# Optimization experiments

Hardware: AMD Instinct MI355X
Metric: run time of the kernel (lower is better)

Reference implementation:

```python
import jax, jax.numpy as jnp
import numpy as np

SYM_LIST = jnp.array([0, 1, 2, 3])  # init kwarg sym_list


def setup_inputs() -> dict:
    key = jax.random.key(0)
    k1, k2, k3, k4 = jax.random.split(key, 4)
    bs, n = 16, 2048
    target = jax.random.normal(k1, (bs, n, 3), dtype=jnp.float32)
    model_points = jax.random.normal(k2, (bs, n, 3), dtype=jnp.float32)
    idx = jax.random.randint(k3, (bs, 1), 0, 8)
    H = jax.random.normal(k4, (bs, 4, 4), dtype=jnp.float32)
    return {"target": target, "model_points": model_points, "idx": idx, "H": H}


def reference(target, model_points, idx, H):
    # base = H[:, :3, :3]^T per batch; pred = model_points @ base + t
    base = jnp.swapaxes(H[:, :3, :3], 1, 2)            # [bs, 3, 3]
    t = H[:, :3, 3][:, None, :]                        # [bs, 1, 3]
    tf = jnp.einsum('bnd,bde->bne', model_points, base) + t  # [bs, N, 3]

    # Squared pairwise distances (argmin-equivalent to L2 norm used in knn()).
    # d2[b, q, r] = ||tf[b,q] - target[b,r]||^2
    d2 = (jnp.sum(tf * tf, axis=-1)[:, :, None]
          + jnp.sum(target * target, axis=-1)[:, None, :]
          - 2.0 * jnp.einsum('bqd,brd->bqr', tf, target))  # [bs, N, N]
    inds = jnp.argmin(d2, axis=2)                      # [bs, N] nearest target per query
    gathered = jnp.take_along_axis(target, inds[:, :, None], axis=1)  # [bs, N, 3]

    # Only symmetric objects (idx in sym_list) get the NN-rearranged target.
    is_sym = jnp.isin(idx[:, 0], SYM_LIST)[:, None, None]  # [bs, 1, 1]
    tgt = jnp.where(is_sym, gathered, target)

    # dis = mean_n ||tf - tgt||_2, per batch element
    dis = jnp.mean(jnp.linalg.norm(tf - tgt, axis=2), axis=1)  # [bs]
    return dis
```

## Files before the change

### kernel.cpp

```cpp
#include <hip/hip_runtime.h>

#define N 2048
#define BS 16
#define QG 256
#define NQG (N / QG)
#define TS 256
#define NTS (N / TS)
#define WAVES 4
#define TPB (WAVES * 64)
#define TPW (TS / WAVES)


__global__ __launch_bounds__(TPB) void addsloss_k1(
    const float* __restrict__ target,
    const float* __restrict__ mp,
    const int* __restrict__ idx,
    const float* __restrict__ H,
    float* __restrict__ wsmin)
{
    __shared__ float4 tlds[TS];
    __shared__ float  pmin[WAVES][QG];

    const int bid  = blockIdx.x;
    const int b    = bid >> 6;
    const int rem  = bid & 63;
    const int qg   = rem >> 3;
    const int ts   = rem & 7;
    const int tid  = threadIdx.x;
    const int wave = tid >> 6;
    const int lane = tid & 63;

    const int  cls = idx[b];
    const bool sym = (cls >= 0) && (cls <= 3);
    if (!sym) return;

    const float* tb = target + (size_t)b * N * 3;
    const float* mb = mp     + (size_t)b * N * 3;
    const float* hb = H      + b * 16;

    {
        const int t = ts * TS + tid;
        const float x = tb[t * 3 + 0];
        const float y = tb[t * 3 + 1];
        const float z = tb[t * 3 + 2];
        tlds[tid] = make_float4(x, y, z, x * x + y * y + z * z);
    }

    float fx[4], fy[4], fz[4];
    #pragma unroll
    for (int qi = 0; qi < 4; ++qi) {
        const int q = qg * QG + qi * 64 + lane;
        const float m0 = mb[q * 3 + 0];
        const float m1 = mb[q * 3 + 1];
        const float m2 = mb[q * 3 + 2];
        fx[qi] = hb[0] * m0 + hb[1]  * m1 + hb[2]  * m2 + hb[3];
        fy[qi] = hb[4] * m0 + hb[5]  * m1 + hb[6]  * m2 + hb[7];
        fz[qi] = hb[8] * m0 + hb[9]  * m1 + hb[10] * m2 + hb[11];
    }

    __syncthreads();

    const float4* t4 = &tlds[wave * TPW];

    float acc[4][4];
    #pragma unroll
    for (int qi = 0; qi < 4; ++qi)
        #pragma unroll
        for (int ti = 0; ti < 4; ++ti) acc[qi][ti] = 3.4e38f;

    for (int j = 0; j < TPW; j += 4) {
        const float4 T0 = t4[j + 0];
        const float4 T1 = t4[j + 1];
        const float4 T2 = t4[j + 2];
        const float4 T3 = t4[j + 3];
        #pragma unroll
        for (int qi = 0; qi < 4; ++qi) {
            float dot;
            dot = T0.x * fx[qi]; dot = fmaf(T0.y, fy[qi], dot); dot = fmaf(T0.z, fz[qi], dot);
            acc[qi][0] = fminf(acc[qi][0], fmaf(dot, -2.0f, T0.w));
            dot = T1.x * fx[qi]; dot = fmaf(T1.y, fy[qi], dot); dot = fmaf(T1.z, fz[qi], dot);
            acc[qi][1] = fminf(acc[qi][1], fmaf(dot, -2.0f, T1.w));
            dot = T2.x * fx[qi]; dot = fmaf(T2.y, fy[qi], dot); dot = fmaf(T2.z, fz[qi], dot);
            acc[qi][2] = fminf(acc[qi][2], fmaf(dot, -2.0f, T2.w));
            dot = T3.x * fx[qi]; dot = fmaf(T3.y, fy[qi], dot); dot = fmaf(T3.z, fz[qi], dot);
            acc[qi][3] = fminf(acc[qi][3], fmaf(dot, -2.0f, T3.w));
        }
    }

    #pragma unroll
    for (int qi = 0; qi < 4; ++qi)
        pmin[wave][qi * 64 + lane] =
            fminf(fminf(acc[qi][0], acc[qi][1]), fminf(acc[qi][2], acc[qi][3]));
    __syncthreads();

    float* wrow = wsmin + ((size_t)(b * NTS + ts)) * N + qg * QG;
    const float m = fminf(fminf(pmin[0][tid], pmin[1][tid]),
                          fminf(pmin[2][tid], pmin[3][tid]));
    wrow[tid] = m;
}

__global__ __launch_bounds__(1024) void addsloss_k2(
    const float* __restrict__ target,
    const float* __restrict__ mp,
    const int* __restrict__ idx,
    const float* __restrict__ H,
    const float* __restrict__ wsmin,
    float* __restrict__ out)
{
    __shared__ float ps[16];
    const int b    = blockIdx.x;
    const int tid  = threadIdx.x;
    const int wave = tid >> 6;
    const int lane = tid & 63;

    const int  cls = idx[b];
    const bool sym = (cls >= 0) && (cls <= 3);

    const float* tb = target + (size_t)b * N * 3;
    const float* mb = mp     + (size_t)b * N * 3;
    const float* hb = H      + b * 16;

    float s = 0.0f;
    #pragma unroll
    for (int k = 0; k < N / 1024; ++k) {
        const int q = k * 1024 + tid;
        const float m0 = mb[q * 3 + 0];
        const float m1 = mb[q * 3 + 1];
        const float m2 = mb[q * 3 + 2];
        const float fx = hb[0] * m0 + hb[1]  * m1 + hb[2]  * m2 + hb[3];
        const float fy = hb[4] * m0 + hb[5]  * m1 + hb[6]  * m2 + hb[7];
        const float fz = hb[8] * m0 + hb[9]  * m1 + hb[10] * m2 + hb[11];

        float d;
        if (sym) {
            float m = 3.4e38f;
            #pragma unroll
            for (int t = 0; t < NTS; ++t)
                m = fminf(m, wsmin[((size_t)(b * NTS + t)) * N + q]);
            const float c = fx * fx + fy * fy + fz * fz;
            d = sqrtf(fmaxf(0.0f, c + m));
        } else {
            const float dx = fx - tb[q * 3 + 0];
            const float dy = fy - tb[q * 3 + 1];
            const float dz = fz - tb[q * 3 + 2];
            d = sqrtf(dx * dx + dy * dy + dz * dz);
        }
        s += d;
    }

    #pragma unroll
    for (int off = 32; off > 0; off >>= 1) s += __shfl_down(s, off);
    if (lane == 0) ps[wave] = s;
    __syncthreads();
    if (tid == 0) {
        float tot = 0.0f;
        #pragma unroll
        for (int w = 0; w < 16; ++w) tot += ps[w];
        out[b] = tot * (1.0f / (float)N);
    }
}

extern "C" void kernel_launch(void* const* d_in, const int* in_sizes, int n_in,
                              void* d_out, int out_size, void* d_ws, size_t ws_size,
                              hipStream_t stream) {
    const float* target = (const float*)d_in[0];
    const float* mp     = (const float*)d_in[1];
    const int*   idx    = (const int*)  d_in[2];
    const float* H      = (const float*)d_in[3];
    float*       out    = (float*)d_out;
    float*       wsmin  = (float*)d_ws;

    addsloss_k1<<<BS * NQG * NTS, TPB, 0, stream>>>(target, mp, idx, H, wsmin);
    addsloss_k2<<<BS, 1024, 0, stream>>>(target, mp, idx, H, wsmin, out);
}
```

Before: 15.51 us.

## Halve target tile to double k1 blocks, fold -2 factor, vectorize k2 loads

The target tile size drops from 256 to 128, which doubles the k1 grid to 2048 blocks so more work runs in parallel across CUs. The -2 scale is folded into the query coordinates so each distance takes three FMAs with no extra multiply, and the inner loop is fully unrolled. k2 now runs 512 threads that each handle 4 queries, using float4 loads for the points and the partial minima. The trade-off is twice as many partial-min rows (16 per query) to write and reduce, plus half-idle threads when staging target points into shared memory.

Measured after the change: 14.58 us. 1.06x faster.

```diff
diff --git a/kernel.cpp b/kernel.cpp
--- a/kernel.cpp
+++ b/kernel.cpp
@@ -4,11 +4,12 @@
 #define BS 16
 #define QG 256
 #define NQG (N / QG)
-#define TS 256
+#define TS 128
 #define NTS (N / TS)
 #define WAVES 4
 #define TPB (WAVES * 64)
 #define TPW (TS / WAVES)
+#define F4I (TPW / 4)
 
 
 __global__ __launch_bounds__(TPB) void addsloss_k1(
@@ -22,10 +23,10 @@
     __shared__ float  pmin[WAVES][QG];
 
     const int bid  = blockIdx.x;
-    const int b    = bid >> 6;
-    const int rem  = bid & 63;
-    const int qg   = rem >> 3;
-    const int ts   = rem & 7;
+    const int b    = bid >> 7;
+    const int rem  = bid & 127;
+    const int qg   = rem >> 4;
+    const int ts   = rem & 15;
     const int tid  = threadIdx.x;
     const int wave = tid >> 6;
     const int lane = tid & 63;
@@ -38,7 +39,7 @@
     const float* mb = mp     + (size_t)b * N * 3;
     const float* hb = H      + b * 16;
 
-    {
+    if (tid < TS) {
         const int t = ts * TS + tid;
         const float x = tb[t * 3 + 0];
         const float y = tb[t * 3 + 1];
@@ -46,16 +47,16 @@
         tlds[tid] = make_float4(x, y, z, x * x + y * y + z * z);
     }
 
-    float fx[4], fy[4], fz[4];
+    float ngx[4], ngy[4], ngz[4];
     #pragma unroll
     for (int qi = 0; qi < 4; ++qi) {
         const int q = qg * QG + qi * 64 + lane;
         const float m0 = mb[q * 3 + 0];
         const float m1 = mb[q * 3 + 1];
         const float m2 = mb[q * 3 + 2];
-        fx[qi] = hb[0] * m0 + hb[1]  * m1 + hb[2]  * m2 + hb[3];
-        fy[qi] = hb[4] * m0 + hb[5]  * m1 + hb[6]  * m2 + hb[7];
-        fz[qi] = hb[8] * m0 + hb[9]  * m1 + hb[10] * m2 + hb[11];
+        ngx[qi] = -2.0f * (hb[0] * m0 + hb[1]  * m1 + hb[2]  * m2 + hb[3]);
+        ngy[qi] = -2.0f * (hb[4] * m0 + hb[5]  * m1 + hb[6]  * m2 + hb[7]);
+        ngz[qi] = -2.0f * (hb[8] * m0 + hb[9]  * m1 + hb[10] * m2 + hb[11]);
     }
 
     __syncthreads();
@@ -68,22 +69,23 @@
         #pragma unroll
         for (int ti = 0; ti < 4; ++ti) acc[qi][ti] = 3.4e38f;
 
-    for (int j = 0; j < TPW; j += 4) {
-        const float4 T0 = t4[j + 0];
-        const float4 T1 = t4[j + 1];
-        const float4 T2 = t4[j + 2];
-        const float4 T3 = t4[j + 3];
+    #pragma unroll
+    for (int j = 0; j < F4I; ++j) {
+        const float4 T0 = t4[j * 4 + 0];
+        const float4 T1 = t4[j * 4 + 1];
+        const float4 T2 = t4[j * 4 + 2];
+        const float4 T3 = t4[j * 4 + 3];
         #pragma unroll
         for (int qi = 0; qi < 4; ++qi) {
-            float dot;
-            dot = T0.x * fx[qi]; dot = fmaf(T0.y, fy[qi], dot); dot = fmaf(T0.z, fz[qi], dot);
-            acc[qi][0] = fminf(acc[qi][0], fmaf(dot, -2.0f, T0.w));
-            dot = T1.x * fx[qi]; dot = fmaf(T1.y, fy[qi], dot); dot = fmaf(T1.z, fz[qi], dot);
-            acc[qi][1] = fminf(acc[qi][1], fmaf(dot, -2.0f, T1.w));
-            dot = T2.x * fx[qi]; dot = fmaf(T2.y, fy[qi], dot); dot = fmaf(T2.z, fz[qi], dot);
-            acc[qi][2] = fminf(acc[qi][2], fmaf(dot, -2.0f, T2.w));
-            dot = T3.x * fx[qi]; dot = fmaf(T3.y, fy[qi], dot); dot = fmaf(T3.z, fz[qi], dot);
-            acc[qi][3] = fminf(acc[qi][3], fmaf(dot, -2.0f, T3.w));
+            float h;
+            h = T0.w; h = fmaf(ngx[qi], T0.x, h); h = fmaf(ngy[qi], T0.y, h);
+            h = fmaf(ngz[qi], T0.z, h); acc[qi][0] = fminf(acc[qi][0], h);
+            h = T1.w; h = fmaf(ngx[qi], T1.x, h); h = fmaf(ngy[qi], T1.y, h);
+            h = fmaf(ngz[qi], T1.z, h); acc[qi][1] = fminf(acc[qi][1], h);
+            h = T2.w; h = fmaf(ngx[qi], T2.x, h); h = fmaf(ngy[qi], T2.y, h);
+            h = fmaf(ngz[qi], T2.z, h); acc[qi][2] = fminf(acc[qi][2], h);
+            h = T3.w; h = fmaf(ngx[qi], T3.x, h); h = fmaf(ngy[qi], T3.y, h);
+            h = fmaf(ngz[qi], T3.z, h); acc[qi][3] = fminf(acc[qi][3], h);
         }
     }
 
@@ -99,7 +101,7 @@
     wrow[tid] = m;
 }
 
-__global__ __launch_bounds__(1024) void addsloss_k2(
+__global__ __launch_bounds__(512) void addsloss_k2(
     const float* __restrict__ target,
     const float* __restrict__ mp,
     const int* __restrict__ idx,
@@ -107,7 +109,7 @@
     const float* __restrict__ wsmin,
     float* __restrict__ out)
 {
-    __shared__ float ps[16];
+    __shared__ float ps[8];
     const int b    = blockIdx.x;
     const int tid  = threadIdx.x;
     const int wave = tid >> 6;
@@ -120,32 +122,51 @@
     const float* mb = mp     + (size_t)b * N * 3;
     const float* hb = H      + b * 16;
 
+    const int q0 = tid * 4;
+
+    const float4* mq = reinterpret_cast<const float4*>(mb + (size_t)q0 * 3);
+    const float4 A = mq[0], B = mq[1], C = mq[2];
+    const float qx[4] = {A.x, A.w, B.z, C.y};
+    const float qy[4] = {A.y, B.x, B.w, C.z};
+    const float qz[4] = {A.z, B.y, C.x, C.w};
+
+    float fx[4], fy[4], fz[4];
+    #pragma unroll
+    for (int i = 0; i < 4; ++i) {
+        fx[i] = hb[0] * qx[i] + hb[1]  * qy[i] + hb[2]  * qz[i] + hb[3];
+        fy[i] = hb[4] * qx[i] + hb[5]  * qy[i] + hb[6]  * qz[i] + hb[7];
+        fz[i] = hb[8] * qx[i] + hb[9]  * qy[i] + hb[10] * qz[i] + hb[11];
+    }
+
     float s = 0.0f;
-    #pragma unroll
-    for (int k = 0; k < N / 1024; ++k) {
-        const int q = k * 1024 + tid;
-        const float m0 = mb[q * 3 + 0];
-        const float m1 = mb[q * 3 + 1];
-        const float m2 = mb[q * 3 + 2];
-        const float fx = hb[0] * m0 + hb[1]  * m1 + hb[2]  * m2 + hb[3];
-        const float fy = hb[4] * m0 + hb[5]  * m1 + hb[6]  * m2 + hb[7];
-        const float fz = hb[8] * m0 + hb[9]  * m1 + hb[10] * m2 + hb[11];
-
-        float d;
-        if (sym) {
-            float m = 3.4e38f;
-            #pragma unroll
-            for (int t = 0; t < NTS; ++t)
-                m = fminf(m, wsmin[((size_t)(b * NTS + t)) * N + q]);
-            const float c = fx * fx + fy * fy + fz * fz;
-            d = sqrtf(fmaxf(0.0f, c + m));
-        } else {
-            const float dx = fx - tb[q * 3 + 0];
-            const float dy = fy - tb[q * 3 + 1];
-            const float dz = fz - tb[q * 3 + 2];
-            d = sqrtf(dx * dx + dy * dy + dz * dz);
+    if (sym) {
+        float4 m = make_float4(3.4e38f, 3.4e38f, 3.4e38f, 3.4e38f);
+        #pragma unroll
+        for (int t = 0; t < NTS; ++t) {
+            const float4 v = *reinterpret_cast<const float4*>(
+                wsmin + ((size_t)(b * NTS + t)) * N + q0);
+            m.x = fminf(m.x, v.x); m.y = fminf(m.y, v.y);
+            m.z = fminf(m.z, v.z); m.w = fminf(m.w, v.w);
         }
-        s += d;
+        const float mm[4] = {m.x, m.y, m.z, m.w};
+        #pragma unroll
+        for (int i = 0; i < 4; ++i) {
+            const float c = fx[i] * fx[i] + fy[i] * fy[i] + fz[i] * fz[i];
+            s += sqrtf(fmaxf(0.0f, c + mm[i]));
+        }
+    } else {
+        const float4* tq = reinterpret_cast<const float4*>(tb + (size_t)q0 * 3);
+        const float4 D = tq[0], E = tq[1], F = tq[2];
+        const float tx[4] = {D.x, D.w, E.z, F.y};
+        const float ty[4] = {D.y, E.x, E.w, F.z};
+        const float tz[4] = {D.z, E.y, F.x, F.w};
+        #pragma unroll
+        for (int i = 0; i < 4; ++i) {
+            const float dx = fx[i] - tx[i];
+            const float dy = fy[i] - ty[i];
+            const float dz = fz[i] - tz[i];
+            s += sqrtf(dx * dx + dy * dy + dz * dz);
+        }
     }
 
     #pragma unroll
@@ -155,7 +176,7 @@
     if (tid == 0) {
         float tot = 0.0f;
         #pragma unroll
-        for (int w = 0; w < 16; ++w) tot += ps[w];
+        for (int w = 0; w < 8; ++w) tot += ps[w];
         out[b] = tot * (1.0f / (float)N);
     }
 }
@@ -171,5 +192,5 @@
     float*       wsmin  = (float*)d_ws;
 
     addsloss_k1<<<BS * NQG * NTS, TPB, 0, stream>>>(target, mp, idx, H, wsmin);
-    addsloss_k2<<<BS, 1024, 0, stream>>>(target, mp, idx, H, wsmin, out);
+    addsloss_k2<<<BS, 512, 0, stream>>>(target, mp, idx, H, wsmin, out);
 }
```

## Retile NN kernel with more queries per lane and split final reduction

Applied to the files above, without the earlier changes.

The nearest-neighbour kernel now keeps eight query points per lane and uses smaller target tiles, so the grid grows to 2048 blocks. The -2 factor is folded into the query coordinates so each distance is a chain of three FMAs, and the inner loop is fully unrolled. The second kernel is split across 8 blocks per batch with a tiny third kernel for the final sum, which spreads the reduction over more CUs. In exchange there is four times as much partial-min workspace to write and read, plus an extra kernel launch.

Result: no change. 15.78 us (+1.7%).

```diff
diff --git a/kernel.cpp b/kernel.cpp
--- a/kernel.cpp
+++ b/kernel.cpp
@@ -2,16 +2,17 @@
 
 #define N 2048
 #define BS 16
-#define QG 256
+#define QG 512
 #define NQG (N / QG)
-#define TS 256
+#define TS 64
 #define NTS (N / TS)
 #define WAVES 4
 #define TPB (WAVES * 64)
 #define TPW (TS / WAVES)
+#define QPL 8
 
 
-__global__ __launch_bounds__(TPB) void addsloss_k1(
+__global__ __launch_bounds__(TPB, 4) void addsloss_k1(
     const float* __restrict__ target,
     const float* __restrict__ mp,
     const int* __restrict__ idx,
@@ -22,10 +23,10 @@
     __shared__ float  pmin[WAVES][QG];
 
     const int bid  = blockIdx.x;
-    const int b    = bid >> 6;
-    const int rem  = bid & 63;
-    const int qg   = rem >> 3;
-    const int ts   = rem & 7;
+    const int b    = bid >> 7;
+    const int rem  = bid & 127;
+    const int qg   = rem >> 5;
+    const int ts   = rem & 31;
     const int tid  = threadIdx.x;
     const int wave = tid >> 6;
     const int lane = tid & 63;
@@ -38,7 +39,7 @@
     const float* mb = mp     + (size_t)b * N * 3;
     const float* hb = H      + b * 16;
 
-    {
+    if (tid < TS) {
         const int t = ts * TS + tid;
         const float x = tb[t * 3 + 0];
         const float y = tb[t * 3 + 1];
@@ -46,72 +47,79 @@
         tlds[tid] = make_float4(x, y, z, x * x + y * y + z * z);
     }
 
-    float fx[4], fy[4], fz[4];
+    float ngx[QPL], ngy[QPL], ngz[QPL];
     #pragma unroll
-    for (int qi = 0; qi < 4; ++qi) {
+    for (int qi = 0; qi < QPL; ++qi) {
         const int q = qg * QG + qi * 64 + lane;
         const float m0 = mb[q * 3 + 0];
         const float m1 = mb[q * 3 + 1];
         const float m2 = mb[q * 3 + 2];
-        fx[qi] = hb[0] * m0 + hb[1]  * m1 + hb[2]  * m2 + hb[3];
-        fy[qi] = hb[4] * m0 + hb[5]  * m1 + hb[6]  * m2 + hb[7];
-        fz[qi] = hb[8] * m0 + hb[9]  * m1 + hb[10] * m2 + hb[11];
+        ngx[qi] = -2.0f * (hb[0] * m0 + hb[1]  * m1 + hb[2]  * m2 + hb[3]);
+        ngy[qi] = -2.0f * (hb[4] * m0 + hb[5]  * m1 + hb[6]  * m2 + hb[7]);
+        ngz[qi] = -2.0f * (hb[8] * m0 + hb[9]  * m1 + hb[10] * m2 + hb[11]);
     }
 
     __syncthreads();
 
     const float4* t4 = &tlds[wave * TPW];
 
-    float acc[4][4];
+    float acc[QPL][4];
     #pragma unroll
-    for (int qi = 0; qi < 4; ++qi)
+    for (int qi = 0; qi < QPL; ++qi)
         #pragma unroll
         for (int ti = 0; ti < 4; ++ti) acc[qi][ti] = 3.4e38f;
 
-    for (int j = 0; j < TPW; j += 4) {
-        const float4 T0 = t4[j + 0];
-        const float4 T1 = t4[j + 1];
-        const float4 T2 = t4[j + 2];
-        const float4 T3 = t4[j + 3];
+    #pragma unroll
+    for (int j = 0; j < TPW / 4; ++j) {
+        const float4 T0 = t4[j * 4 + 0];
+        const float4 T1 = t4[j * 4 + 1];
+        const float4 T2 = t4[j * 4 + 2];
+        const float4 T3 = t4[j * 4 + 3];
         #pragma unroll
-        for (int qi = 0; qi < 4; ++qi) {
-            float dot;
-            dot = T0.x * fx[qi]; dot = fmaf(T0.y, fy[qi], dot); dot = fmaf(T0.z, fz[qi], dot);
-            acc[qi][0] = fminf(acc[qi][0], fmaf(dot, -2.0f, T0.w));
-            dot = T1.x * fx[qi]; dot = fmaf(T1.y, fy[qi], dot); dot = fmaf(T1.z, fz[qi], dot);
-            acc[qi][1] = fminf(acc[qi][1], fmaf(dot, -2.0f, T1.w));
-            dot = T2.x * fx[qi]; dot = fmaf(T2.y, fy[qi], dot); dot = fmaf(T2.z, fz[qi], dot);
-            acc[qi][2] = fminf(acc[qi][2], fmaf(dot, -2.0f, T2.w));
-            dot = T3.x * fx[qi]; dot = fmaf(T3.y, fy[qi], dot); dot = fmaf(T3.z, fz[qi], dot);
-            acc[qi][3] = fminf(acc[qi][3], fmaf(dot, -2.0f, T3.w));
+        for (int qi = 0; qi < QPL; ++qi) {
+            float h;
+            h = T0.w; h = fmaf(ngx[qi], T0.x, h); h = fmaf(ngy[qi], T0.y, h);
+            h = fmaf(ngz[qi], T0.z, h); acc[qi][0] = fminf(acc[qi][0], h);
+            h = T1.w; h = fmaf(ngx[qi], T1.x, h); h = fmaf(ngy[qi], T1.y, h);
+            h = fmaf(ngz[qi], T1.z, h); acc[qi][1] = fminf(acc[qi][1], h);
+            h = T2.w; h = fmaf(ngx[qi], T2.x, h); h = fmaf(ngy[qi], T2.y, h);
+            h = fmaf(ngz[qi], T2.z, h); acc[qi][2] = fminf(acc[qi][2], h);
+            h = T3.w; h = fmaf(ngx[qi], T3.x, h); h = fmaf(ngy[qi], T3.y, h);
+            h = fmaf(ngz[qi], T3.z, h); acc[qi][3] = fminf(acc[qi][3], h);
         }
     }
 
     #pragma unroll
-    for (int qi = 0; qi < 4; ++qi)
+    for (int qi = 0; qi < QPL; ++qi)
         pmin[wave][qi * 64 + lane] =
             fminf(fminf(acc[qi][0], acc[qi][1]), fminf(acc[qi][2], acc[qi][3]));
     __syncthreads();
 
     float* wrow = wsmin + ((size_t)(b * NTS + ts)) * N + qg * QG;
-    const float m = fminf(fminf(pmin[0][tid], pmin[1][tid]),
-                          fminf(pmin[2][tid], pmin[3][tid]));
-    wrow[tid] = m;
+    #pragma unroll
+    for (int k = 0; k < QG / TPB; ++k) {
+        const int i = k * TPB + tid;
+        wrow[i] = fminf(fminf(pmin[0][i], pmin[1][i]),
+                        fminf(pmin[2][i], pmin[3][i]));
+    }
 }
 
-__global__ __launch_bounds__(1024) void addsloss_k2(
+__global__ __launch_bounds__(256) void addsloss_k2(
     const float* __restrict__ target,
     const float* __restrict__ mp,
     const int* __restrict__ idx,
     const float* __restrict__ H,
     const float* __restrict__ wsmin,
-    float* __restrict__ out)
+    float* __restrict__ ws2)
 {
-    __shared__ float ps[16];
-    const int b    = blockIdx.x;
+    __shared__ float ps[4];
+    const int bid  = blockIdx.x;
+    const int b    = bid >> 3;
+    const int part = bid & 7;
     const int tid  = threadIdx.x;
     const int wave = tid >> 6;
     const int lane = tid & 63;
+    const int q    = part * 256 + tid;
 
     const int  cls = idx[b];
     const bool sym = (cls >= 0) && (cls <= 3);
@@ -120,43 +128,44 @@
     const float* mb = mp     + (size_t)b * N * 3;
     const float* hb = H      + b * 16;
 
-    float s = 0.0f;
-    #pragma unroll
-    for (int k = 0; k < N / 1024; ++k) {
-        const int q = k * 1024 + tid;
-        const float m0 = mb[q * 3 + 0];
-        const float m1 = mb[q * 3 + 1];
-        const float m2 = mb[q * 3 + 2];
-        const float fx = hb[0] * m0 + hb[1]  * m1 + hb[2]  * m2 + hb[3];
-        const float fy = hb[4] * m0 + hb[5]  * m1 + hb[6]  * m2 + hb[7];
-        const float fz = hb[8] * m0 + hb[9]  * m1 + hb[10] * m2 + hb[11];
+    const float m0 = mb[q * 3 + 0];
+    const float m1 = mb[q * 3 + 1];
+    const float m2 = mb[q * 3 + 2];
+    const float fx = hb[0] * m0 + hb[1]  * m1 + hb[2]  * m2 + hb[3];
+    const float fy = hb[4] * m0 + hb[5]  * m1 + hb[6]  * m2 + hb[7];
+    const float fz = hb[8] * m0 + hb[9]  * m1 + hb[10] * m2 + hb[11];
 
-        float d;
-        if (sym) {
-            float m = 3.4e38f;
-            #pragma unroll
-            for (int t = 0; t < NTS; ++t)
-                m = fminf(m, wsmin[((size_t)(b * NTS + t)) * N + q]);
-            const float c = fx * fx + fy * fy + fz * fz;
-            d = sqrtf(fmaxf(0.0f, c + m));
-        } else {
-            const float dx = fx - tb[q * 3 + 0];
-            const float dy = fy - tb[q * 3 + 1];
-            const float dz = fz - tb[q * 3 + 2];
-            d = sqrtf(dx * dx + dy * dy + dz * dz);
-        }
-        s += d;
+    float d;
+    if (sym) {
+        float m = 3.4e38f;
+        #pragma unroll
+        for (int t = 0; t < NTS; ++t)
+            m = fminf(m, wsmin[((size_t)(b * NTS + t)) * N + q]);
+        const float c = fx * fx + fy * fy + fz * fz;
+        d = sqrtf(fmaxf(0.0f, c + m));
+    } else {
+        const float dx = fx - tb[q * 3 + 0];
+        const float dy = fy - tb[q * 3 + 1];
+        const float dz = fz - tb[q * 3 + 2];
+        d = sqrtf(dx * dx + dy * dy + dz * dz);
     }
 
     #pragma unroll
-    for (int off = 32; off > 0; off >>= 1) s += __shfl_down(s, off);
-    if (lane == 0) ps[wave] = s;
+    for (int off = 32; off > 0; off >>= 1) d += __shfl_down(d, off);
+    if (lane == 0) ps[wave] = d;
     __syncthreads();
-    if (tid == 0) {
-        float tot = 0.0f;
+    if (tid == 0) ws2[bid] = ps[0] + ps[1] + ps[2] + ps[3];
+}
+
+__global__ __launch_bounds__(64) void addsloss_k3(
+    const float* __restrict__ ws2, float* __restrict__ out)
+{
+    const int b = threadIdx.x;
+    if (b < BS) {
+        float s = 0.0f;
         #pragma unroll
-        for (int w = 0; w < 16; ++w) tot += ps[w];
-        out[b] = tot * (1.0f / (float)N);
+        for (int p = 0; p < 8; ++p) s += ws2[b * 8 + p];
+        out[b] = s * (1.0f / (float)N);
     }
 }
 
@@ -169,7 +178,9 @@
     const float* H      = (const float*)d_in[3];
     float*       out    = (float*)d_out;
     float*       wsmin  = (float*)d_ws;
+    float*       ws2    = wsmin + (size_t)BS * NTS * N;
 
     addsloss_k1<<<BS * NQG * NTS, TPB, 0, stream>>>(target, mp, idx, H, wsmin);
-    addsloss_k2<<<BS, 1024, 0, stream>>>(target, mp, idx, H, wsmin, out);
+    addsloss_k2<<<BS * 8, 256, 0, stream>>>(target, mp, idx, H, wsmin, ws2);
+    addsloss_k3<<<1, 64, 0, stream>>>(ws2, out);
 }
```
